# Kernel tuning notes

Measured on AMD Instinct MI355X. Metric: run time of the kernel, lower is better.

The kernel has to match this reference:

```python
import jax, jax.numpy as jnp
import numpy as np

TOTAL = 16_000_000
NUM_SAMPLES = 200
K = 100

def setup_inputs() -> dict:
    key = jax.random.key(0)
    k1, k2, k3, k4 = jax.random.split(key, 4)
    y = jax.random.normal(k1, (TOTAL,), dtype=jnp.float32)
    mu = jax.random.normal(k2, (TOTAL,), dtype=jnp.float32)
    std = jax.random.uniform(k3, (TOTAL,), dtype=jnp.float32, minval=0.1, maxval=1.0)
    idx = jax.random.randint(k4, (NUM_SAMPLES, K), 0, TOTAL, dtype=jnp.int64 if jax.config.jax_enable_x64 else jnp.int32)
    return {"y": y, "mu": mu, "std": std, "idx": idx}

def reference(y, mu, std, idx):
    # Gather all 200 samples of K=100 elements in one pass: [num_samples, K]
    sy, smu, sstd = y[idx], mu[idx], std[idx]
    # Chi-square statistic per sample
    q = jnp.sum(((sy - smu) / sstd) ** 2, axis=-1)  # [num_samples]
    emp_mu = jnp.mean(q)
    emp_var = jnp.var(q, ddof=1)  # torch .var() is unbiased
    k = jnp.float32(idx.shape[1])
    two_k = 2.0 * k  # true variance of chi-square with K dof
    # KL( N(emp_mu, sqrt(emp_var)) || N(K, sqrt(2K)) )
    kl = 0.5 * jnp.log(two_k / emp_var) + (emp_var + (emp_mu - k) ** 2) / (2.0 * two_k) - 0.5
    return kl
```

## Files before the change

kernel.cpp:

```cpp
#include <hip/hip_runtime.h>
#include <hip/hip_bf16.h>
#include <math.h>


#define NUM_SAMPLES 200
#define KDOF 100

__device__ __forceinline__ float wave_reduce_sum(float v) {
    for (int off = 32; off > 0; off >>= 1)
        v += __shfl_down(v, off, 64);
    return v;
}

__global__ void __launch_bounds__(128) compute_q_kernel(
        const float* __restrict__ y, const float* __restrict__ mu,
        const float* __restrict__ sd, const int* __restrict__ idx,
        float* __restrict__ q) {
    const int i = blockIdx.x;
    const int j = threadIdx.x;
    float term = 0.0f;
    if (j < KDOF) {
        const int id = idx[i * KDOF + j];
        const float d = (y[id] - mu[id]) / sd[id];
        term = d * d;
    }
    term = wave_reduce_sum(term);
    __shared__ float partial[2];
    const int wave = j >> 6;
    if ((j & 63) == 0) partial[wave] = term;
    __syncthreads();
    if (j == 0) q[i] = partial[0] + partial[1];
}

__global__ void __launch_bounds__(256) finalize_kernel(
        const float* __restrict__ q, float* __restrict__ out) {
    const int t = threadIdx.x;
    const int wave = t >> 6;
    const int lane = t & 63;
    __shared__ float lds[4];
    __shared__ float s_mean;

    const float v = (t < NUM_SAMPLES) ? q[t] : 0.0f;

    float s = wave_reduce_sum(v);
    if (lane == 0) lds[wave] = s;
    __syncthreads();
    if (t == 0) {
        float tot = lds[0] + lds[1] + lds[2] + lds[3];
        s_mean = tot / (float)NUM_SAMPLES;
    }
    __syncthreads();
    const float mean = s_mean;

    const float d = (t < NUM_SAMPLES) ? (v - mean) : 0.0f;
    float ss = wave_reduce_sum(d * d);
    __syncthreads();
    if (lane == 0) lds[wave] = ss;
    __syncthreads();
    if (t == 0) {
        const float ssd = lds[0] + lds[1] + lds[2] + lds[3];
        const float var = ssd / (float)(NUM_SAMPLES - 1);
        const float k = (float)KDOF;
        const float two_k = 2.0f * k;
        const float dm = mean - k;
        const float kl = 0.5f * logf(two_k / var) + (var + dm * dm) / (2.0f * two_k) - 0.5f;
        out[0] = kl;
    }
}

extern "C" void kernel_launch(void* const* d_in, const int* in_sizes, int n_in,
                              void* d_out, int out_size, void* d_ws, size_t ws_size,
                              hipStream_t stream) {
    const float* y   = (const float*)d_in[0];
    const float* mu  = (const float*)d_in[1];
    const float* sd  = (const float*)d_in[2];
    const int*   idx = (const int*)d_in[3];
    float* out = (float*)d_out;
    float* q   = (float*)d_ws;

    compute_q_kernel<<<NUM_SAMPLES, 128, 0, stream>>>(y, mu, sd, idx, q);
    finalize_kernel<<<1, 256, 0, stream>>>(q, out);
}
```

Baseline: 149.0 us.

## Fuse finalize into chi-square kernel via atomic accumulation and last-block reduction

Removes the separate finalize kernel launch. Each block atomically adds its q and q^2 into a workspace accumulator, and the last block to arrive (detected with an atomic counter) computes the mean, variance and KL. A memset is added to zero the accumulator. Computing the variance as sumsq minus n*mean^2 in fp32 risks catastrophic cancellation when q is around 100, and atomic float ordering makes the result nondeterministic.

```diff
diff --git a/kernel.cpp b/kernel.cpp
--- a/kernel.cpp
+++ b/kernel.cpp
@@ -6,65 +6,51 @@
 #define NUM_SAMPLES 200
 #define KDOF 100
 
-__device__ __forceinline__ float wave_reduce_sum(float v) {
-    for (int off = 32; off > 0; off >>= 1)
-        v += __shfl_down(v, off, 64);
-    return v;
-}
+struct Accum {
+    float sum;
+    float sumsq;
+    unsigned int count;
+};
 
-__global__ void __launch_bounds__(128) compute_q_kernel(
+__global__ void __launch_bounds__(128) fused_chi2_kl_kernel(
         const float* __restrict__ y, const float* __restrict__ mu,
         const float* __restrict__ sd, const int* __restrict__ idx,
-        float* __restrict__ q) {
+        float* __restrict__ out, Accum* __restrict__ acc) {
     const int i = blockIdx.x;
     const int j = threadIdx.x;
+
     float term = 0.0f;
     if (j < KDOF) {
         const int id = idx[i * KDOF + j];
         const float d = (y[id] - mu[id]) / sd[id];
         term = d * d;
     }
-    term = wave_reduce_sum(term);
+    for (int off = 32; off > 0; off >>= 1)
+        term += __shfl_down(term, off, 64);
+
     __shared__ float partial[2];
-    const int wave = j >> 6;
-    if ((j & 63) == 0) partial[wave] = term;
+    if ((j & 63) == 0) partial[j >> 6] = term;
     __syncthreads();
-    if (j == 0) q[i] = partial[0] + partial[1];
-}
 
-__global__ void __launch_bounds__(256) finalize_kernel(
-        const float* __restrict__ q, float* __restrict__ out) {
-    const int t = threadIdx.x;
-    const int wave = t >> 6;
-    const int lane = t & 63;
-    __shared__ float lds[4];
-    __shared__ float s_mean;
-
-    const float v = (t < NUM_SAMPLES) ? q[t] : 0.0f;
-
-    float s = wave_reduce_sum(v);
-    if (lane == 0) lds[wave] = s;
-    __syncthreads();
-    if (t == 0) {
-        float tot = lds[0] + lds[1] + lds[2] + lds[3];
-        s_mean = tot / (float)NUM_SAMPLES;
-    }
-    __syncthreads();
-    const float mean = s_mean;
-
-    const float d = (t < NUM_SAMPLES) ? (v - mean) : 0.0f;
-    float ss = wave_reduce_sum(d * d);
-    __syncthreads();
-    if (lane == 0) lds[wave] = ss;
-    __syncthreads();
-    if (t == 0) {
-        const float ssd = lds[0] + lds[1] + lds[2] + lds[3];
-        const float var = ssd / (float)(NUM_SAMPLES - 1);
-        const float k = (float)KDOF;
-        const float two_k = 2.0f * k;
-        const float dm = mean - k;
-        const float kl = 0.5f * logf(two_k / var) + (var + dm * dm) / (2.0f * two_k) - 0.5f;
-        out[0] = kl;
+    if (j == 0) {
+        const float q = partial[0] + partial[1];
+        atomicAdd(&acc->sum, q);
+        atomicAdd(&acc->sumsq, q * q);
+        __threadfence();
+        const unsigned int old = atomicAdd(&acc->count, 1u);
+        if (old == NUM_SAMPLES - 1) {
+            __threadfence();
+            const float s  = atomicAdd(&acc->sum, 0.0f);
+            const float ss = atomicAdd(&acc->sumsq, 0.0f);
+            const float n = (float)NUM_SAMPLES;
+            const float mean = s / n;
+            const float var = (ss - n * mean * mean) / (n - 1.0f);
+            const float k = (float)KDOF;
+            const float two_k = 2.0f * k;
+            const float dm = mean - k;
+            out[0] = 0.5f * logf(two_k / var)
+                   + (var + dm * dm) / (2.0f * two_k) - 0.5f;
+        }
     }
 }
 
@@ -76,8 +62,8 @@
     const float* sd  = (const float*)d_in[2];
     const int*   idx = (const int*)d_in[3];
     float* out = (float*)d_out;
-    float* q   = (float*)d_ws;
+    Accum* acc = (Accum*)d_ws;
 
-    compute_q_kernel<<<NUM_SAMPLES, 128, 0, stream>>>(y, mu, sd, idx, q);
-    finalize_kernel<<<1, 256, 0, stream>>>(q, out);
+    hipMemsetAsync(acc, 0, sizeof(Accum), stream);
+    fused_chi2_kl_kernel<<<NUM_SAMPLES, 128, 0, stream>>>(y, mu, sd, idx, out, acc);
 }
```

After: 157.7 us. 5.9% more time.
